# Performance work log

Measured on AMD Instinct MI355X. Metric: run time of the kernel, lower is better.

## Reference

```python
import jax, jax.numpy as jnp
import numpy as np

B, N, D, E = 4, 1024, 1024, 8
TOP_N = 2
THRESHOLD = 0.2
EPS = 1e-9
CAP_FACTOR = 2.0
MIN_EXPERT_CAPACITY = 4
H = int(D * 4 * 2 / 3)  # GEGLU hidden = 2730


def setup_inputs() -> dict:
    key = jax.random.key(0)
    ks = jax.random.split(key, 8)
    u = lambda k, shape, fan: jax.random.uniform(k, shape, jnp.float32, -1.0, 1.0) * (fan ** -0.5)
    return {
        "x": jax.random.normal(ks[0], (B, N, D), jnp.float32),
        "route_probs": jax.random.uniform(ks[1], (TOP_N, B, N), jnp.float32),
        "gate_w": u(ks[2], (D, E), D),
        "w1": u(ks[3], (E, D, 2 * H), 2 * H),
        "b1": u(ks[4], (E, 2 * H), 2 * H),
        "mult_bias": jnp.ones((E, H), jnp.float32),
        "w2": u(ks[5], (E, H, D), D),
        "b2": u(ks[6], (E, D), D),
    }


def reference(x, route_probs, gate_w, w1, b1, mult_bias, w2, b2):
    b, n, d = x.shape
    e = gate_w.shape[1]
    cap = max(min(n, int(n * CAP_FACTOR / e)), MIN_EXPERT_CAPACITY)  # 256

    # ---- top-n gating ----
    logits = jnp.einsum('bnd,de->bne', x, gate_w)
    raw_gates = jax.nn.softmax(logits, axis=-1)
    gate_vals, gate_idx = jax.lax.top_k(raw_gates, TOP_N)          # [b,n,k]
    gate_vals = jnp.moveaxis(gate_vals, -1, 0)                      # [k,b,n]
    gate_idx = jnp.moveaxis(gate_idx, -1, 0)                        # [k,b,n]
    one_hot_idx = jax.nn.one_hot(gate_idx, e, dtype=x.dtype)        # [k,b,n,e]

    denom = jnp.clip(gate_vals.sum(axis=0, keepdims=True), EPS)
    gate_vals = gate_vals / denom

    # route to expert k>0 with prob min(1, gate/threshold); expert 0 always routed
    should_route = route_probs < (gate_vals / THRESHOLD)
    should_route = should_route.at[0].set(True)
    mask = one_hot_idx * should_route[..., None].astype(x.dtype)    # [k,b,n,e]

    # exclusive cumsum over sequence dim -> position within each expert
    mask_cumsum = jnp.cumsum(mask, axis=2) - mask                   # [k,b,n,e]

    positions, masks = [], []
    prev_count = jnp.zeros((b, 1, e), x.dtype)
    for k in range(TOP_N):  # small fixed loop over top-n
        pos_e = (mask_cumsum[k] + prev_count) * mask[k]             # [b,n,e]
        mk = mask[k] * (pos_e < float(cap)).astype(x.dtype)
        prev_count = prev_count + mk.sum(axis=1, keepdims=True)
        positions.append(pos_e.sum(axis=-1))                        # [b,n]
        masks.append(mk)
    positions = jnp.stack(positions)                                # [k,b,n]
    mask = jnp.stack(masks)                                         # [k,b,n,e]

    mask_flat = mask.sum(axis=-1)                                   # [k,b,n] in {0,1}
    gates = gate_vals * mask_flat
    pos_one_hot = jax.nn.one_hot(positions.astype(jnp.int32), cap, dtype=x.dtype)  # [k,b,n,c]

    # combine tensor [b,n,e,c]; dispatch is its boolean support
    combine = jnp.einsum('kbn,kbne,kbnc->bnec', gates * mask_flat, one_hot_idx, pos_one_hot)
    dispatch = (combine > 0).astype(x.dtype)

    # ---- dispatch tokens to experts ----
    xe = jnp.einsum('bnd,bnec->ebcd', x, dispatch)                  # [e,b,c,d]

    # ---- per-expert GEGLU FFN (grouped GEMM) ----
    h = jnp.einsum('ebcd,edf->ebcf', xe, w1) + b1[:, None, None, :]
    val, gate = jnp.split(h, 2, axis=-1)
    act = jax.nn.gelu(gate, approximate=False) * val * mult_bias[:, None, None, :]
    out_e = jnp.einsum('ebch,ehd->ebcd', act, w2) + b2[:, None, None, :]

    # ---- combine ----
    out = jnp.einsum('ebcd,bnec->bnd', out_e, combine)
    return out


if __name__ == '__main__':
    inp = setup_inputs()
    o = reference(**inp)
    print(o.shape, o.dtype)
```

## Files before the change

### kernel.cpp

```cpp
#include <hip/hip_runtime.h>
#include <hip/hip_bf16.h>
#include <math.h>

#define B_ 4
#define N_ 1024
#define D_ 1024
#define E_ 8
#define H_ 2730
#define H2_ 5460
#define CAP_ 256
#define NTOK 4096
#define NSLOT 8192
#define NKT1 16
#define NKT2 43
#define NFG 22

typedef __attribute__((ext_vector_type(8))) short short8;
typedef __attribute__((ext_vector_type(4))) float f32x4;

__device__ __forceinline__ unsigned short f2bf(float f) {
    __hip_bfloat16 h = __float2bfloat16(f);
    return *reinterpret_cast<unsigned short*>(&h);
}
__device__ __forceinline__ float bf2f(unsigned short u) {
    unsigned x = ((unsigned)u) << 16;
    union { unsigned u; float f; } c; c.u = x; return c.f;
}

#define GLL16(g, l)                                                          \
    __builtin_amdgcn_global_load_lds(                                        \
        (const __attribute__((address_space(1))) void*)(g),                  \
        (__attribute__((address_space(3))) void*)(l), 16, 0, 0)

#define VMCNT4() asm volatile("s_waitcnt vmcnt(4)" ::: "memory")
#define VMCNT3() asm volatile("s_waitcnt vmcnt(3)" ::: "memory")
#define VMCNT0() asm volatile("s_waitcnt vmcnt(0)" ::: "memory")
#define SBAR()   __builtin_amdgcn_s_barrier()
#define SCHEDB() __builtin_amdgcn_sched_barrier(0)
#define MFMA16(a, b, c) __builtin_amdgcn_mfma_f32_16x16x32_bf16((a), (b), (c), 0, 0, 0)


__global__ __launch_bounds__(256) void k_cvt1(const float* __restrict__ w1,
                                              unsigned short* __restrict__ w1p) {
    const int fg = blockIdx.x;
    const int kt = blockIdx.y;
    const int e  = blockIdx.z;
    const float* w1e = w1 + (size_t)e * D_ * H2_;
    unsigned short* dst = w1p + (((size_t)((e * NFG + fg) * NKT1 + kt)) << 14);
#pragma unroll
    for (int i = 0; i < 8; ++i) {
        const int o = i * 256 + threadIdx.x;
        const int l = o & 63, n16 = (o >> 6) & 15, k32 = o >> 10;
        const int f = fg * 128 + ((n16 & 7) << 4) + (l & 15);
        const int k = kt * 64 + (k32 << 5) + ((l >> 4) << 3);
        ushort4 r0 = {0, 0, 0, 0}, r1 = {0, 0, 0, 0};
        if (f < H_) {
            const float* s = w1e + (size_t)k * H2_ + (n16 >= 8 ? H_ : 0) + f;
            r0.x = f2bf(s[0]);
            r0.y = f2bf(s[(size_t)H2_]);
            r0.z = f2bf(s[(size_t)2 * H2_]);
            r0.w = f2bf(s[(size_t)3 * H2_]);
            r1.x = f2bf(s[(size_t)4 * H2_]);
            r1.y = f2bf(s[(size_t)5 * H2_]);
            r1.z = f2bf(s[(size_t)6 * H2_]);
            r1.w = f2bf(s[(size_t)7 * H2_]);
        }
        *reinterpret_cast<ushort4*>(dst + (size_t)o * 8) = r0;
        *reinterpret_cast<ushort4*>(dst + (size_t)o * 8 + 4) = r1;
    }
}

__global__ __launch_bounds__(256) void k_cvt2(const float* __restrict__ w2,
                                              unsigned short* __restrict__ w2p) {
    const int kt = blockIdx.x;
    const int nt = blockIdx.y;
    const int e  = blockIdx.z;
    const float* w2e = w2 + (size_t)e * H_ * D_;
    unsigned short* dst = w2p + (((size_t)((e * 8 + nt) * NKT2 + kt)) << 13);
#pragma unroll
    for (int i = 0; i < 4; ++i) {
        const int o = i * 256 + threadIdx.x;
        const int l = o & 63, n16 = (o >> 6) & 7, k32 = o >> 9;
        const int d = nt * 128 + (n16 << 4) + (l & 15);
        const int f = kt * 64 + (k32 << 5) + ((l >> 4) << 3);
        const float* s = w2e + (size_t)f * D_ + d;
        ushort4 r0, r1;
        r0.x = (f + 0 < H_) ? f2bf(s[0]) : 0;
        r0.y = (f + 1 < H_) ? f2bf(s[(size_t)D_]) : 0;
        r0.z = (f + 2 < H_) ? f2bf(s[(size_t)2 * D_]) : 0;
        r0.w = (f + 3 < H_) ? f2bf(s[(size_t)3 * D_]) : 0;
        r1.x = (f + 4 < H_) ? f2bf(s[(size_t)4 * D_]) : 0;
        r1.y = (f + 5 < H_) ? f2bf(s[(size_t)5 * D_]) : 0;
        r1.z = (f + 6 < H_) ? f2bf(s[(size_t)6 * D_]) : 0;
        r1.w = (f + 7 < H_) ? f2bf(s[(size_t)7 * D_]) : 0;
        *reinterpret_cast<ushort4*>(dst + (size_t)o * 8) = r0;
        *reinterpret_cast<ushort4*>(dst + (size_t)o * 8 + 4) = r1;
    }
}

__global__ __launch_bounds__(256) void k_gate(const float* __restrict__ x,
                                              const float* __restrict__ route,
                                              const float* __restrict__ gw,
                                              int* __restrict__ tokE,
                                              float* __restrict__ tokG,
                                              int* __restrict__ tokR) {
    const int wave = threadIdx.x >> 6, lane = threadIdx.x & 63;
    const int t = blockIdx.x * 4 + wave;
    float acc[E_];
#pragma unroll
    for (int e = 0; e < E_; ++e) acc[e] = 0.f;
    const float* xr = x + (size_t)t * D_;
    for (int d = lane; d < D_; d += 64) {
        float xv = xr[d];
        const float* g = gw + d * E_;
#pragma unroll
        for (int e = 0; e < E_; ++e) acc[e] = fmaf(xv, g[e], acc[e]);
    }
#pragma unroll
    for (int e = 0; e < E_; ++e) {
#pragma unroll
        for (int off = 32; off; off >>= 1) acc[e] += __shfl_xor(acc[e], off);
    }
    if (lane == 0) {
        float m = acc[0];
#pragma unroll
        for (int e = 1; e < E_; ++e) m = fmaxf(m, acc[e]);
        float p[E_]; float s = 0.f;
#pragma unroll
        for (int e = 0; e < E_; ++e) { p[e] = expf(acc[e] - m); s += p[e]; }
        int i0 = 0; float v0 = p[0];
#pragma unroll
        for (int e = 1; e < E_; ++e) if (p[e] > v0) { v0 = p[e]; i0 = e; }
        int i1 = (i0 == 0) ? 1 : 0; float v1 = p[i1];
#pragma unroll
        for (int e = 0; e < E_; ++e) if (e != i0 && p[e] > v1) { v1 = p[e]; i1 = e; }
        float p0 = v0 / s, p1 = v1 / s;
        float denom = fmaxf(p0 + p1, 1e-9f);
        float g0 = p0 / denom, g1 = p1 / denom;
        int r1 = route[NTOK + t] < (g1 / 0.2f);
        tokE[t] = i0; tokE[NTOK + t] = i1;
        tokG[t] = g0; tokG[NTOK + t] = g1;
        tokR[t] = r1;
    }
}

__global__ __launch_bounds__(256) void k_pos(const int* __restrict__ tokE,
                                             const float* __restrict__ tokG,
                                             const int* __restrict__ tokR,
                                             int* __restrict__ sot,
                                             int* __restrict__ tos) {
    const int e = blockIdx.x & 7, b = blockIdx.x >> 3;
    const int t = threadIdx.x;
    __shared__ int sc[256];
    const int base_bt = b * N_ + t * 4;
    int m0[4], m1[4];
    int c0 = 0, c1 = 0;
#pragma unroll
    for (int i = 0; i < 4; ++i) {
        int bt = base_bt + i;
        m0[i] = (tokE[bt] == e) ? 1 : 0;
        m1[i] = ((tokE[NTOK + bt] == e) && tokR[bt]) ? 1 : 0;
        c0 += m0[i]; c1 += m1[i];
    }
    int packed = c0 | (c1 << 16);
    sc[t] = packed;
    __syncthreads();
    for (int off = 1; off < 256; off <<= 1) {
        int v = (t >= off) ? sc[t - off] : 0;
        __syncthreads();
        sc[t] += v;
        __syncthreads();
    }
    int incl = sc[t];
    int total = sc[255];
    int excl = incl - packed;
    int base0 = excl & 0xffff;
    int base1 = excl >> 16;
    int kept0 = min(total & 0xffff, CAP_);
#pragma unroll
    for (int i = 0; i < 4; ++i) {
        int bt = base_bt + i;
        if (m0[i]) {
            int pos = base0++;
            if (pos < CAP_ && tokG[bt] > 0.f) {
                int s = ((e * B_ + b) << 8) + pos;
                sot[bt] = s;
                tos[s] = bt;
            }
        }
        if (m1[i]) {
            int pos = (base1++) + kept0;
            if (pos < CAP_ && tokG[NTOK + bt] > 0.f) {
                int s = ((e * B_ + b) << 8) + pos;
                sot[NTOK + bt] = s;
                tos[s] = bt;
            }
        }
    }
}

__global__ __launch_bounds__(256) void k_disp(const float* __restrict__ x,
                                              const int* __restrict__ tos,
                                              unsigned short* __restrict__ xeP) {
    const int t = threadIdx.x;
    const int s = blockIdx.x * 2 + (t >> 7);
    const int q = t & 127;
    const int bt = tos[s];
    const int kt = q >> 3, k32 = (q >> 2) & 1, kq = q & 3;
    const int lane = (kq << 4) | (s & 15);
    const int m16 = (s >> 4) & 15;
    const int sgrp = s >> 8;
    unsigned short* dst = xeP + (((size_t)(sgrp * NKT1 + kt)) << 14) + (k32 << 13) + (m16 << 9) + lane * 8;
    ushort4 r0 = {0, 0, 0, 0}, r1 = {0, 0, 0, 0};
    if (bt >= 0) {
        const float4 v0 = *reinterpret_cast<const float4*>(x + ((size_t)bt << 10) + q * 8);
        const float4 v1 = *reinterpret_cast<const float4*>(x + ((size_t)bt << 10) + q * 8 + 4);
        r0.x = f2bf(v0.x); r0.y = f2bf(v0.y); r0.z = f2bf(v0.z); r0.w = f2bf(v0.w);
        r1.x = f2bf(v1.x); r1.y = f2bf(v1.y); r1.z = f2bf(v1.z); r1.w = f2bf(v1.w);
    }
    *reinterpret_cast<ushort4*>(dst) = r0;
    *reinterpret_cast<ushort4*>(dst + 4) = r1;
}

#define LDF(BUF, idx) (*reinterpret_cast<const short8*>(&BUF[(idx) * 512 + lane8]))

#define FFN1_MM03(AF0, AF1, AF2, AF3)                                         \
    do {                                                                      \
        acc[0][0]=MFMA16(AF0,bf0,acc[0][0]); acc[0][1]=MFMA16(AF0,bf1,acc[0][1]); \
        acc[0][2]=MFMA16(AF0,bf2,acc[0][2]); acc[0][3]=MFMA16(AF0,bf3,acc[0][3]); \
        acc[1][0]=MFMA16(AF1,bf0,acc[1][0]); acc[1][1]=MFMA16(AF1,bf1,acc[1][1]); \
        acc[1][2]=MFMA16(AF1,bf2,acc[1][2]); acc[1][3]=MFMA16(AF1,bf3,acc[1][3]); \
        acc[2][0]=MFMA16(AF2,bf0,acc[2][0]); acc[2][1]=MFMA16(AF2,bf1,acc[2][1]); \
        acc[2][2]=MFMA16(AF2,bf2,acc[2][2]); acc[2][3]=MFMA16(AF2,bf3,acc[2][3]); \
        acc[3][0]=MFMA16(AF3,bf0,acc[3][0]); acc[3][1]=MFMA16(AF3,bf1,acc[3][1]); \
        acc[3][2]=MFMA16(AF3,bf2,acc[3][2]); acc[3][3]=MFMA16(AF3,bf3,acc[3][3]); \
    } while (0)
#define FFN1_MM47(AF0, AF1, AF2, AF3)                                         \
    do {                                                                      \
        acc[4][0]=MFMA16(AF0,bf0,acc[4][0]); acc[4][1]=MFMA16(AF0,bf1,acc[4][1]); \
        acc[4][2]=MFMA16(AF0,bf2,acc[4][2]); acc[4][3]=MFMA16(AF0,bf3,acc[4][3]); \
        acc[5][0]=MFMA16(AF1,bf0,acc[5][0]); acc[5][1]=MFMA16(AF1,bf1,acc[5][1]); \
        acc[5][2]=MFMA16(AF1,bf2,acc[5][2]); acc[5][3]=MFMA16(AF1,bf3,acc[5][3]); \
        acc[6][0]=MFMA16(AF2,bf0,acc[6][0]); acc[6][1]=MFMA16(AF2,bf1,acc[6][1]); \
        acc[6][2]=MFMA16(AF2,bf2,acc[6][2]); acc[6][3]=MFMA16(AF2,bf3,acc[6][3]); \
        acc[7][0]=MFMA16(AF3,bf0,acc[7][0]); acc[7][1]=MFMA16(AF3,bf1,acc[7][1]); \
        acc[7][2]=MFMA16(AF3,bf2,acc[7][2]); acc[7][3]=MFMA16(AF3,bf3,acc[7][3]); \
    } while (0)

#define FFN1_KT(ARD, BRD, AWR, BWR, KTN, PF)                                  \
    do {                                                                      \
        const unsigned short* asn = abase + ((size_t)(KTN) << 14);            \
        const unsigned short* bsn = bbase + ((size_t)(KTN) << 14);            \
        short8 af0, af1, af2, af3, bf0, bf1, bf2, bf3;                        \
        SCHEDB(); VMCNT4(); SBAR(); SCHEDB();                                 \
        if (PF) {                                                             \
            GLL16(asn + woff + lane8, (char*)&AWR[woff]);                     \
            GLL16(asn + woff + 512 + lane8, (char*)&AWR[woff + 512]);         \
        }                                                                     \
        bf0 = LDF(BRD, bn0); bf1 = LDF(BRD, bn0 + 1);                         \
        bf2 = LDF(BRD, bn0 + 8); bf3 = LDF(BRD, bn0 + 9);                     \
        af0 = LDF(ARD, am0 + 0); af1 = LDF(ARD, am0 + 1);                     \
        af2 = LDF(ARD, am0 + 2); af3 = LDF(ARD, am0 + 3);                     \
        __builtin_amdgcn_s_setprio(1);                                        \
        FFN1_MM03(af0, af1, af2, af3);                                        \
        __builtin_amdgcn_s_setprio(0);                                        \
        if (PF) {                                                             \
            GLL16(bsn + woff + lane8, (char*)&BWR[woff]);                     \
            GLL16(bsn + woff + 512 + lane8, (char*)&BWR[woff + 512]);         \
        }                                                                     \
        af0 = LDF(ARD, am0 + 4); af1 = LDF(ARD, am0 + 5);                     \
        af2 = LDF(ARD, am0 + 6); af3 = LDF(ARD, am0 + 7);                     \
        __builtin_amdgcn_s_setprio(1);                                        \
        FFN1_MM47(af0, af1, af2, af3);                                        \
        __builtin_amdgcn_s_setprio(0);                                        \
        SCHEDB(); if (PF) { VMCNT4(); } else { VMCNT0(); } SBAR(); SCHEDB();  \
        if (PF) {                                                             \
            GLL16(asn + 8192 + woff + lane8, (char*)&AWR[8192 + woff]);       \
            GLL16(asn + 8192 + woff + 512 + lane8, (char*)&AWR[8192 + woff + 512]); \
        }                                                                     \
        bf0 = LDF(BRD, 16 + bn0); bf1 = LDF(BRD, 16 + bn0 + 1);               \
        bf2 = LDF(BRD, 16 + bn0 + 8); bf3 = LDF(BRD, 16 + bn0 + 9);           \
        af0 = LDF(ARD, 16 + am0 + 0); af1 = LDF(ARD, 16 + am0 + 1);           \
        af2 = LDF(ARD, 16 + am0 + 2); af3 = LDF(ARD, 16 + am0 + 3);           \
        __builtin_amdgcn_s_setprio(1);                                        \
        FFN1_MM03(af0, af1, af2, af3);                                        \
        __builtin_amdgcn_s_setprio(0);                                        \
        if (PF) {                                                             \
            GLL16(bsn + 8192 + woff + lane8, (char*)&BWR[8192 + woff]);       \
            GLL16(bsn + 8192 + woff + 512 + lane8, (char*)&BWR[8192 + woff + 512]); \
        }                                                                     \
        af0 = LDF(ARD, 16 + am0 + 4); af1 = LDF(ARD, 16 + am0 + 5);           \
        af2 = LDF(ARD, 16 + am0 + 6); af3 = LDF(ARD, 16 + am0 + 7);           \
        __builtin_amdgcn_s_setprio(1);                                        \
        FFN1_MM47(af0, af1, af2, af3);                                        \
        __builtin_amdgcn_s_setprio(0);                                        \
    } while (0)

__global__ __launch_bounds__(512) void k_ffn1(const unsigned short* __restrict__ xeP,
                                              const unsigned short* __restrict__ w1p,
                                              const float* __restrict__ b1,
                                              const float* __restrict__ mbias,
                                              unsigned short* __restrict__ actP) {
    const int wg = blockIdx.x;
    const int e = wg & 7;
    const int rem = wg >> 3;
    const int fg = rem >> 2;
    const int rt = rem & 3;
    const int sgrp = e * 4 + rt;

    __shared__ unsigned short Ab0[16384];
    __shared__ unsigned short Bb0[16384];
    __shared__ unsigned short Ab1[16384];
    __shared__ unsigned short Bb1[16384];

    const int tid = threadIdx.x, lane = tid & 63, w = tid >> 6;
    const int wm = w >> 2, wn = w & 3;
    const int lane8 = lane * 8;
    const int woff = w * 1024;
    const int am0 = wm * 8, bn0 = wn * 2;

    const unsigned short* abase = xeP + ((size_t)(sgrp * NKT1) << 14);
    const unsigned short* bbase = w1p + ((size_t)((e * NFG + fg) * NKT1) << 14);

    f32x4 acc[8][4];
#pragma unroll
    for (int i = 0; i < 8; ++i)
#pragma unroll
        for (int j = 0; j < 4; ++j) acc[i][j] = (f32x4)(0.f);

    GLL16(abase + woff + lane8, (char*)&Ab0[woff]);
    GLL16(abase + woff + 512 + lane8, (char*)&Ab0[woff + 512]);
    GLL16(bbase + woff + lane8, (char*)&Bb0[woff]);
    GLL16(bbase + woff + 512 + lane8, (char*)&Bb0[woff + 512]);
    GLL16(abase + 8192 + woff + lane8, (char*)&Ab0[8192 + woff]);
    GLL16(abase + 8192 + woff + 512 + lane8, (char*)&Ab0[8192 + woff + 512]);
    GLL16(bbase + 8192 + woff + lane8, (char*)&Bb0[8192 + woff]);
    GLL16(bbase + 8192 + woff + 512 + lane8, (char*)&Bb0[8192 + woff + 512]);

    for (int kt = 0; kt < NKT1; kt += 2) {
        FFN1_KT(Ab0, Bb0, Ab1, Bb1, kt + 1, 1);
        FFN1_KT(Ab1, Bb1, Ab0, Bb0, kt + 2, (kt + 2) < NKT1);
    }

    const float* b1e = b1 + (size_t)e * H2_;
    const float* mbe = mbias + (size_t)e * H_;
    const int colL = lane & 15, rq4 = (lane >> 4) * 4;
#pragma unroll
    for (int mi = 0; mi < 8; ++mi) {
        const int Rl = wm * 128 + mi * 16 + rq4;
#pragma unroll
        for (int vi = 0; vi < 2; ++vi) {
            const int f = fg * 128 + wn * 32 + vi * 16 + colL;
            if (f >= NKT2 * 64) continue;
            const bool real = f < H_;
            const float bv = real ? b1e[f] : 0.f;
            const float bg = real ? b1e[H_ + f] : 0.f;
            const float mv = real ? mbe[f] : 0.f;
            const int ktf = f >> 6, k32f = (f >> 5) & 1;
            const int lhi = ((f >> 3) & 3) << 4;
            const int bb = f & 7;
            const size_t cbase = ((size_t)(sgrp * NKT2 + ktf) << 14) + (k32f << 13);
#pragma unroll
            for (int j = 0; j < 4; ++j) {
                const int R = Rl + j;
                float a = 0.f;
                if (real) {
                    const float val = acc[mi][vi][j] + bv;
                    const float gt  = acc[mi][2 + vi][j] + bg;
                    a = 0.5f * gt * (1.f + erff(gt * 0.70710678118654752f)) * val * mv;
                }
                actP[cbase + ((R >> 4) << 9) + (size_t)((lhi | (R & 15)) * 8 + bb)] = f2bf(a);
            }
        }
    }
}

#define FFN2_MM03(AF0, AF1, AF2, AF3)                                         \
    do {                                                                      \
        acc[0][0]=MFMA16(AF0,bf0,acc[0][0]); acc[0][1]=MFMA16(AF0,bf1,acc[0][1]); \
        acc[1][0]=MFMA16(AF1,bf0,acc[1][0]); acc[1][1]=MFMA16(AF1,bf1,acc[1][1]); \
        acc[2][0]=MFMA16(AF2,bf0,acc[2][0]); acc[2][1]=MFMA16(AF2,bf1,acc[2][1]); \
        acc[3][0]=MFMA16(AF3,bf0,acc[3][0]); acc[3][1]=MFMA16(AF3,bf1,acc[3][1]); \
    } while (0)
#define FFN2_MM47(AF0, AF1, AF2, AF3)                                         \
    do {                                                                      \
        acc[4][0]=MFMA16(AF0,bf0,acc[4][0]); acc[4][1]=MFMA16(AF0,bf1,acc[4][1]); \
        acc[5][0]=MFMA16(AF1,bf0,acc[5][0]); acc[5][1]=MFMA16(AF1,bf1,acc[5][1]); \
        acc[6][0]=MFMA16(AF2,bf0,acc[6][0]); acc[6][1]=MFMA16(AF2,bf1,acc[6][1]); \
        acc[7][0]=MFMA16(AF3,bf0,acc[7][0]); acc[7][1]=MFMA16(AF3,bf1,acc[7][1]); \
    } while (0)

#define FFN2_KT(ARD, BRD, AWR, BWR, KTN, PF)                                  \
    do {                                                                      \
        const unsigned short* asn = abase + ((size_t)(KTN) << 14);            \
        const unsigned short* bsn = bbase + ((size_t)(KTN) << 13);            \
        short8 af0, af1, af2, af3, bf0, bf1;                                  \
        SCHEDB(); VMCNT3(); SBAR(); SCHEDB();                                 \
        if (PF) {                                                             \
            GLL16(asn + woff + lane8, (char*)&AWR[woff]);                     \
            GLL16(asn + woff + 512 + lane8, (char*)&AWR[woff + 512]);         \
        }                                                                     \
        bf0 = LDF(BRD, bn0); bf1 = LDF(BRD, bn0 + 1);                         \
        af0 = LDF(ARD, am0 + 0); af1 = LDF(ARD, am0 + 1);                     \
        af2 = LDF(ARD, am0 + 2); af3 = LDF(ARD, am0 + 3);                     \
        __builtin_amdgcn_s_setprio(1);                                        \
        FFN2_MM03(af0, af1, af2, af3);                                        \
        __builtin_amdgcn_s_setprio(0);                                        \
        if (PF) { GLL16(bsn + woffb + lane8, (char*)&BWR[woffb]); }           \
        af0 = LDF(ARD, am0 + 4); af1 = LDF(ARD, am0 + 5);                     \
        af2 = LDF(ARD, am0 + 6); af3 = LDF(ARD, am0 + 7);                     \
        __builtin_amdgcn_s_setprio(1);                                        \
        FFN2_MM47(af0, af1, af2, af3);                                        \
        __builtin_amdgcn_s_setprio(0);                                        \
        SCHEDB(); if (PF) { VMCNT3(); } else { VMCNT0(); } SBAR(); SCHEDB();  \
        if (PF) {                                                             \
            GLL16(asn + 8192 + woff + lane8, (char*)&AWR[8192 + woff]);       \
            GLL16(asn + 8192 + woff + 512 + lane8, (char*)&AWR[8192 + woff + 512]); \
        }                                                                     \
        bf0 = LDF(BRD, 8 + bn0); bf1 = LDF(BRD, 8 + bn0 + 1);                 \
        af0 = LDF(ARD, 16 + am0 + 0); af1 = LDF(ARD, 16 + am0 + 1);           \
        af2 = LDF(ARD, 16 + am0 + 2); af3 = LDF(ARD, 16 + am0 + 3);           \
        __builtin_amdgcn_s_setprio(1);                                        \
        FFN2_MM03(af0, af1, af2, af3);                                        \
        __builtin_amdgcn_s_setprio(0);                                        \
        if (PF) { GLL16(bsn + 4096 + woffb + lane8, (char*)&BWR[4096 + woffb]); } \
        af0 = LDF(ARD, 16 + am0 + 4); af1 = LDF(ARD, 16 + am0 + 5);           \
        af2 = LDF(ARD, 16 + am0 + 6); af3 = LDF(ARD, 16 + am0 + 7);           \
        __builtin_amdgcn_s_setprio(1);                                        \
        FFN2_MM47(af0, af1, af2, af3);                                        \
        __builtin_amdgcn_s_setprio(0);                                        \
    } while (0)

__global__ __launch_bounds__(512) void k_ffn2(const unsigned short* __restrict__ actP,
                                              const unsigned short* __restrict__ w2p,
                                              const float* __restrict__ b2,
                                              unsigned short* __restrict__ oute) {
    const int wg = blockIdx.x;
    const int e = wg & 7;
    const int rem = wg >> 3;
    const int nt = rem >> 2;
    const int mt = rem & 3;
    const int sgrp = e * 4 + mt;

    __shared__ unsigned short Ab0[16384];
    __shared__ unsigned short Bb0[8192];
    __shared__ unsigned short Ab1[16384];
    __shared__ unsigned short Bb1[8192];

    const int tid = threadIdx.x, lane = tid & 63, w = tid >> 6;
    const int wm = w >> 2, wn = w & 3;
    const int lane8 = lane * 8;
    const int woff = w * 1024;
    const int woffb = w * 512;
    const int am0 = wm * 8, bn0 = wn * 2;

    const unsigned short* abase = actP + ((size_t)(sgrp * NKT2) << 14);
    const unsigned short* bbase = w2p + ((size_t)((e * 8 + nt) * NKT2) << 13);

    f32x4 acc[8][2];
#pragma unroll
    for (int i = 0; i < 8; ++i)
#pragma unroll
        for (int j = 0; j < 2; ++j) acc[i][j] = (f32x4)(0.f);

    GLL16(abase + woff + lane8, (char*)&Ab0[woff]);
    GLL16(abase + woff + 512 + lane8, (char*)&Ab0[woff + 512]);
    GLL16(bbase + woffb + lane8, (char*)&Bb0[woffb]);
    GLL16(abase + 8192 + woff + lane8, (char*)&Ab0[8192 + woff]);
    GLL16(abase + 8192 + woff + 512 + lane8, (char*)&Ab0[8192 + woff + 512]);
    GLL16(bbase + 4096 + woffb + lane8, (char*)&Bb0[4096 + woffb]);

    for (int kt = 0; kt < NKT2 - 1; kt += 2) {
        FFN2_KT(Ab0, Bb0, Ab1, Bb1, kt + 1, 1);
        FFN2_KT(Ab1, Bb1, Ab0, Bb0, kt + 2, (kt + 2) < NKT2);
    }
    FFN2_KT(Ab0, Bb0, Ab1, Bb1, NKT2, 0);

    const float* b2e = b2 + (size_t)e * D_;
    const int colL = lane & 15, rq4 = (lane >> 4) * 4;
#pragma unroll
    for (int mi = 0; mi < 8; ++mi) {
#pragma unroll
        for (int vi = 0; vi < 2; ++vi) {
            const int d = nt * 128 + wn * 32 + vi * 16 + colL;
            const float bb2 = b2e[d];
#pragma unroll
            for (int j = 0; j < 4; ++j) {
                const int R = mt * 256 + wm * 128 + mi * 16 + rq4 + j;
                oute[((size_t)(e * 1024 + R) << 10) + d] = f2bf(acc[mi][vi][j] + bb2);
            }
        }
    }
}

__global__ __launch_bounds__(256) void k_comb(const unsigned short* __restrict__ oute,
                                              const int* __restrict__ sot,
                                              const float* __restrict__ tokG,
                                              float* __restrict__ out) {
    const int bt = blockIdx.x;
    const int t = threadIdx.x;
    const int s0 = sot[bt], s1 = sot[NTOK + bt];
    const float g0 = tokG[bt], g1 = tokG[NTOK + bt];
    float r0 = 0.f, r1 = 0.f, r2 = 0.f, r3 = 0.f;
    if (s0 >= 0) {
        const ushort4 v = *reinterpret_cast<const ushort4*>(oute + ((size_t)s0 << 10) + t * 4);
        r0 += g0 * bf2f(v.x); r1 += g0 * bf2f(v.y); r2 += g0 * bf2f(v.z); r3 += g0 * bf2f(v.w);
    }
    if (s1 >= 0) {
        const ushort4 v = *reinterpret_cast<const ushort4*>(oute + ((size_t)s1 << 10) + t * 4);
        r0 += g1 * bf2f(v.x); r1 += g1 * bf2f(v.y); r2 += g1 * bf2f(v.z); r3 += g1 * bf2f(v.w);
    }
    float4 o; o.x = r0; o.y = r1; o.z = r2; o.w = r3;
    *reinterpret_cast<float4*>(out + ((size_t)bt << 10) + t * 4) = o;
}

extern "C" void kernel_launch(void* const* d_in, const int* in_sizes, int n_in,
                              void* d_out, int out_size, void* d_ws, size_t ws_size,
                              hipStream_t stream) {
    const float* x     = (const float*)d_in[0];
    const float* route = (const float*)d_in[1];
    const float* gw    = (const float*)d_in[2];
    const float* w1    = (const float*)d_in[3];
    const float* b1    = (const float*)d_in[4];
    const float* mb    = (const float*)d_in[5];
    const float* w2    = (const float*)d_in[6];
    const float* b2    = (const float*)d_in[7];
    float* out = (float*)d_out;

    char* ws = (char*)d_ws;
    int*   tokE = (int*)(ws + 0);
    float* tokG = (float*)(ws + 32768);
    int*   tokR = (int*)(ws + 65536);
    int*   sot  = (int*)(ws + 81920);
    int*   tos  = (int*)(ws + 114688);
    unsigned short* xeP  = (unsigned short*)(ws + 147456);
    unsigned short* actP = (unsigned short*)(ws + 16924672);
    unsigned short* w1p  = (unsigned short*)(ws + 62013440);
    unsigned short* w2p  = (unsigned short*)(ws + 62013440);
    unsigned short* oute = (unsigned short*)(ws + 107102208);

    hipMemsetAsync(sot, 0xFF, 65536, stream);

    k_cvt1<<<dim3(NFG, NKT1, 8), 256, 0, stream>>>(w1, w1p);
    k_gate<<<NTOK / 4, 256, 0, stream>>>(x, route, gw, tokE, tokG, tokR);
    k_pos<<<E_ * B_, 256, 0, stream>>>(tokE, tokG, tokR, sot, tos);
    k_disp<<<NSLOT / 2, 256, 0, stream>>>(x, tos, xeP);
    k_ffn1<<<704, 512, 0, stream>>>(xeP, w1p, b1, mb, actP);
    k_cvt2<<<dim3(NKT2, 8, 8), 256, 0, stream>>>(w2, w2p);
    k_ffn2<<<256, 512, 0, stream>>>(actP, w2p, b2, oute);
    k_comb<<<NTOK, 256, 0, stream>>>(oute, sot, tokG, out);
}
```

Baseline: 325.6 us.

## Halve FFN GEMM M-tiles to 128 rows with 256-thread blocks

```diff
diff --git a/kernel.cpp b/kernel.cpp
--- a/kernel.cpp
+++ b/kernel.cpp
@@ -12,6 +12,7 @@
 #define NTOK 4096
 #define NSLOT 8192
 #define NKT1 16
+#define NK1T 32
 #define NKT2 43
 #define NFG 22
 
@@ -32,8 +33,6 @@
         (const __attribute__((address_space(1))) void*)(g),                  \
         (__attribute__((address_space(3))) void*)(l), 16, 0, 0)
 
-#define VMCNT4() asm volatile("s_waitcnt vmcnt(4)" ::: "memory")
-#define VMCNT3() asm volatile("s_waitcnt vmcnt(3)" ::: "memory")
 #define VMCNT0() asm volatile("s_waitcnt vmcnt(0)" ::: "memory")
 #define SBAR()   __builtin_amdgcn_s_barrier()
 #define SCHEDB() __builtin_amdgcn_sched_barrier(0)
@@ -224,79 +223,48 @@
 
 #define LDF(BUF, idx) (*reinterpret_cast<const short8*>(&BUF[(idx) * 512 + lane8]))
 
-#define FFN1_MM03(AF0, AF1, AF2, AF3)                                         \
+#define F1TILE(ARD, BRD, AWR, BWR, KTN, PF)                                   \
     do {                                                                      \
-        acc[0][0]=MFMA16(AF0,bf0,acc[0][0]); acc[0][1]=MFMA16(AF0,bf1,acc[0][1]); \
-        acc[0][2]=MFMA16(AF0,bf2,acc[0][2]); acc[0][3]=MFMA16(AF0,bf3,acc[0][3]); \
-        acc[1][0]=MFMA16(AF1,bf0,acc[1][0]); acc[1][1]=MFMA16(AF1,bf1,acc[1][1]); \
-        acc[1][2]=MFMA16(AF1,bf2,acc[1][2]); acc[1][3]=MFMA16(AF1,bf3,acc[1][3]); \
-        acc[2][0]=MFMA16(AF2,bf0,acc[2][0]); acc[2][1]=MFMA16(AF2,bf1,acc[2][1]); \
-        acc[2][2]=MFMA16(AF2,bf2,acc[2][2]); acc[2][3]=MFMA16(AF2,bf3,acc[2][3]); \
-        acc[3][0]=MFMA16(AF3,bf0,acc[3][0]); acc[3][1]=MFMA16(AF3,bf1,acc[3][1]); \
-        acc[3][2]=MFMA16(AF3,bf2,acc[3][2]); acc[3][3]=MFMA16(AF3,bf3,acc[3][3]); \
-    } while (0)
-#define FFN1_MM47(AF0, AF1, AF2, AF3)                                         \
-    do {                                                                      \
-        acc[4][0]=MFMA16(AF0,bf0,acc[4][0]); acc[4][1]=MFMA16(AF0,bf1,acc[4][1]); \
-        acc[4][2]=MFMA16(AF0,bf2,acc[4][2]); acc[4][3]=MFMA16(AF0,bf3,acc[4][3]); \
-        acc[5][0]=MFMA16(AF1,bf0,acc[5][0]); acc[5][1]=MFMA16(AF1,bf1,acc[5][1]); \
-        acc[5][2]=MFMA16(AF1,bf2,acc[5][2]); acc[5][3]=MFMA16(AF1,bf3,acc[5][3]); \
-        acc[6][0]=MFMA16(AF2,bf0,acc[6][0]); acc[6][1]=MFMA16(AF2,bf1,acc[6][1]); \
-        acc[6][2]=MFMA16(AF2,bf2,acc[6][2]); acc[6][3]=MFMA16(AF2,bf3,acc[6][3]); \
-        acc[7][0]=MFMA16(AF3,bf0,acc[7][0]); acc[7][1]=MFMA16(AF3,bf1,acc[7][1]); \
-        acc[7][2]=MFMA16(AF3,bf2,acc[7][2]); acc[7][3]=MFMA16(AF3,bf3,acc[7][3]); \
-    } while (0)
-
-#define FFN1_KT(ARD, BRD, AWR, BWR, KTN, PF)                                  \
-    do {                                                                      \
-        const unsigned short* asn = abase + ((size_t)(KTN) << 14);            \
-        const unsigned short* bsn = bbase + ((size_t)(KTN) << 14);            \
-        short8 af0, af1, af2, af3, bf0, bf1, bf2, bf3;                        \
-        SCHEDB(); VMCNT4(); SBAR(); SCHEDB();                                 \
+        VMCNT0(); SBAR(); SCHEDB();                                           \
         if (PF) {                                                             \
-            GLL16(asn + woff + lane8, (char*)&AWR[woff]);                     \
-            GLL16(asn + woff + 512 + lane8, (char*)&AWR[woff + 512]);         \
+            const unsigned short* as = abase + ((size_t)(KTN) << 13);         \
+            const unsigned short* bs = bbase + ((size_t)(KTN) << 13);         \
+            GLL16(as + t8, (char*)&AWR[wb]);                                  \
+            GLL16(as + 2048 + t8, (char*)&AWR[2048 + wb]);                    \
+            GLL16(bs + t8, (char*)&BWR[wb]);                                  \
+            GLL16(bs + 2048 + t8, (char*)&BWR[2048 + wb]);                    \
+            GLL16(bs + 4096 + t8, (char*)&BWR[4096 + wb]);                    \
+            GLL16(bs + 6144 + t8, (char*)&BWR[6144 + wb]);                    \
         }                                                                     \
-        bf0 = LDF(BRD, bn0); bf1 = LDF(BRD, bn0 + 1);                         \
-        bf2 = LDF(BRD, bn0 + 8); bf3 = LDF(BRD, bn0 + 9);                     \
+        SCHEDB();                                                             \
+        short8 af0, af1, af2, af3, b0, b1, b2, b3, b4, b5, b6, b7;            \
         af0 = LDF(ARD, am0 + 0); af1 = LDF(ARD, am0 + 1);                     \
         af2 = LDF(ARD, am0 + 2); af3 = LDF(ARD, am0 + 3);                     \
+        b0 = LDF(BRD, bn0 + 0); b1 = LDF(BRD, bn0 + 1);                       \
+        b2 = LDF(BRD, bn0 + 2); b3 = LDF(BRD, bn0 + 3);                       \
+        b4 = LDF(BRD, 8 + bn0 + 0); b5 = LDF(BRD, 8 + bn0 + 1);               \
+        b6 = LDF(BRD, 8 + bn0 + 2); b7 = LDF(BRD, 8 + bn0 + 3);               \
         __builtin_amdgcn_s_setprio(1);                                        \
-        FFN1_MM03(af0, af1, af2, af3);                                        \
-        __builtin_amdgcn_s_setprio(0);                                        \
-        if (PF) {                                                             \
-            GLL16(bsn + woff + lane8, (char*)&BWR[woff]);                     \
-            GLL16(bsn + woff + 512 + lane8, (char*)&BWR[woff + 512]);         \
-        }                                                                     \
-        af0 = LDF(ARD, am0 + 4); af1 = LDF(ARD, am0 + 5);                     \
-        af2 = LDF(ARD, am0 + 6); af3 = LDF(ARD, am0 + 7);                     \
-        __builtin_amdgcn_s_setprio(1);                                        \
-        FFN1_MM47(af0, af1, af2, af3);                                        \
-        __builtin_amdgcn_s_setprio(0);                                        \
-        SCHEDB(); if (PF) { VMCNT4(); } else { VMCNT0(); } SBAR(); SCHEDB();  \
-        if (PF) {                                                             \
-            GLL16(asn + 8192 + woff + lane8, (char*)&AWR[8192 + woff]);       \
-            GLL16(asn + 8192 + woff + 512 + lane8, (char*)&AWR[8192 + woff + 512]); \
-        }                                                                     \
-        bf0 = LDF(BRD, 16 + bn0); bf1 = LDF(BRD, 16 + bn0 + 1);               \
-        bf2 = LDF(BRD, 16 + bn0 + 8); bf3 = LDF(BRD, 16 + bn0 + 9);           \
-        af0 = LDF(ARD, 16 + am0 + 0); af1 = LDF(ARD, 16 + am0 + 1);           \
-        af2 = LDF(ARD, 16 + am0 + 2); af3 = LDF(ARD, 16 + am0 + 3);           \
-        __builtin_amdgcn_s_setprio(1);                                        \
-        FFN1_MM03(af0, af1, af2, af3);                                        \
-        __builtin_amdgcn_s_setprio(0);                                        \
-        if (PF) {                                                             \
-            GLL16(bsn + 8192 + woff + lane8, (char*)&BWR[8192 + woff]);       \
-            GLL16(bsn + 8192 + woff + 512 + lane8, (char*)&BWR[8192 + woff + 512]); \
-        }                                                                     \
-        af0 = LDF(ARD, 16 + am0 + 4); af1 = LDF(ARD, 16 + am0 + 5);           \
-        af2 = LDF(ARD, 16 + am0 + 6); af3 = LDF(ARD, 16 + am0 + 7);           \
-        __builtin_amdgcn_s_setprio(1);                                        \
-        FFN1_MM47(af0, af1, af2, af3);                                        \
+        acc[0][0]=MFMA16(af0,b0,acc[0][0]); acc[0][1]=MFMA16(af0,b1,acc[0][1]); \
+        acc[0][2]=MFMA16(af0,b2,acc[0][2]); acc[0][3]=MFMA16(af0,b3,acc[0][3]); \
+        acc[0][4]=MFMA16(af0,b4,acc[0][4]); acc[0][5]=MFMA16(af0,b5,acc[0][5]); \
+        acc[0][6]=MFMA16(af0,b6,acc[0][6]); acc[0][7]=MFMA16(af0,b7,acc[0][7]); \
+        acc[1][0]=MFMA16(af1,b0,acc[1][0]); acc[1][1]=MFMA16(af1,b1,acc[1][1]); \
+        acc[1][2]=MFMA16(af1,b2,acc[1][2]); acc[1][3]=MFMA16(af1,b3,acc[1][3]); \
+        acc[1][4]=MFMA16(af1,b4,acc[1][4]); acc[1][5]=MFMA16(af1,b5,acc[1][5]); \
+        acc[1][6]=MFMA16(af1,b6,acc[1][6]); acc[1][7]=MFMA16(af1,b7,acc[1][7]); \
+        acc[2][0]=MFMA16(af2,b0,acc[2][0]); acc[2][1]=MFMA16(af2,b1,acc[2][1]); \
+        acc[2][2]=MFMA16(af2,b2,acc[2][2]); acc[2][3]=MFMA16(af2,b3,acc[2][3]); \
+        acc[2][4]=MFMA16(af2,b4,acc[2][4]); acc[2][5]=MFMA16(af2,b5,acc[2][5]); \
+        acc[2][6]=MFMA16(af2,b6,acc[2][6]); acc[2][7]=MFMA16(af2,b7,acc[2][7]); \
+        acc[3][0]=MFMA16(af3,b0,acc[3][0]); acc[3][1]=MFMA16(af3,b1,acc[3][1]); \
+        acc[3][2]=MFMA16(af3,b2,acc[3][2]); acc[3][3]=MFMA16(af3,b3,acc[3][3]); \
+        acc[3][4]=MFMA16(af3,b4,acc[3][4]); acc[3][5]=MFMA16(af3,b5,acc[3][5]); \
+        acc[3][6]=MFMA16(af3,b6,acc[3][6]); acc[3][7]=MFMA16(af3,b7,acc[3][7]); \
         __builtin_amdgcn_s_setprio(0);                                        \
     } while (0)
 
-__global__ __launch_bounds__(512) void k_ffn1(const unsigned short* __restrict__ xeP,
+__global__ __launch_bounds__(256) void k_ffn1(const unsigned short* __restrict__ xeP,
                                               const unsigned short* __restrict__ w1p,
                                               const float* __restrict__ b1,
                                               const float* __restrict__ mbias,
@@ -304,53 +272,55 @@
     const int wg = blockIdx.x;
     const int e = wg & 7;
     const int rem = wg >> 3;
-    const int fg = rem >> 2;
-    const int rt = rem & 3;
-    const int sgrp = e * 4 + rt;
-
-    __shared__ unsigned short Ab0[16384];
-    __shared__ unsigned short Bb0[16384];
-    __shared__ unsigned short Ab1[16384];
-    __shared__ unsigned short Bb1[16384];
+    const int fg = rem >> 3;
+    const int rt = rem & 7;
+    const int sgrp = e * 4 + (rt >> 1);
+    const int half = rt & 1;
+
+    __shared__ unsigned short Ab0[4096];
+    __shared__ unsigned short Bb0[8192];
+    __shared__ unsigned short Ab1[4096];
+    __shared__ unsigned short Bb1[8192];
 
     const int tid = threadIdx.x, lane = tid & 63, w = tid >> 6;
-    const int wm = w >> 2, wn = w & 3;
+    const int wm = w >> 1, wn = w & 1;
     const int lane8 = lane * 8;
-    const int woff = w * 1024;
-    const int am0 = wm * 8, bn0 = wn * 2;
-
-    const unsigned short* abase = xeP + ((size_t)(sgrp * NKT1) << 14);
+    const int t8 = tid * 8;
+    const int wb = w * 512;
+    const int am0 = wm * 4, bn0 = wn * 4;
+
+    const unsigned short* abase = xeP + ((size_t)(sgrp * NKT1) << 14) + half * 4096;
     const unsigned short* bbase = w1p + ((size_t)((e * NFG + fg) * NKT1) << 14);
 
-    f32x4 acc[8][4];
-#pragma unroll
-    for (int i = 0; i < 8; ++i)
-#pragma unroll
-        for (int j = 0; j < 4; ++j) acc[i][j] = (f32x4)(0.f);
-
-    GLL16(abase + woff + lane8, (char*)&Ab0[woff]);
-    GLL16(abase + woff + 512 + lane8, (char*)&Ab0[woff + 512]);
-    GLL16(bbase + woff + lane8, (char*)&Bb0[woff]);
-    GLL16(bbase + woff + 512 + lane8, (char*)&Bb0[woff + 512]);
-    GLL16(abase + 8192 + woff + lane8, (char*)&Ab0[8192 + woff]);
-    GLL16(abase + 8192 + woff + 512 + lane8, (char*)&Ab0[8192 + woff + 512]);
-    GLL16(bbase + 8192 + woff + lane8, (char*)&Bb0[8192 + woff]);
-    GLL16(bbase + 8192 + woff + 512 + lane8, (char*)&Bb0[8192 + woff + 512]);
-
-    for (int kt = 0; kt < NKT1; kt += 2) {
-        FFN1_KT(Ab0, Bb0, Ab1, Bb1, kt + 1, 1);
-        FFN1_KT(Ab1, Bb1, Ab0, Bb0, kt + 2, (kt + 2) < NKT1);
+    f32x4 acc[4][8];
+#pragma unroll
+    for (int i = 0; i < 4; ++i)
+#pragma unroll
+        for (int j = 0; j < 8; ++j) acc[i][j] = (f32x4)(0.f);
+
+    GLL16(abase + t8, (char*)&Ab0[wb]);
+    GLL16(abase + 2048 + t8, (char*)&Ab0[2048 + wb]);
+    GLL16(bbase + t8, (char*)&Bb0[wb]);
+    GLL16(bbase + 2048 + t8, (char*)&Bb0[2048 + wb]);
+    GLL16(bbase + 4096 + t8, (char*)&Bb0[4096 + wb]);
+    GLL16(bbase + 6144 + t8, (char*)&Bb0[6144 + wb]);
+
+    for (int kt = 0; kt < NK1T; kt += 2) {
+        F1TILE(Ab0, Bb0, Ab1, Bb1, kt + 1, 1);
+        F1TILE(Ab1, Bb1, Ab0, Bb0, kt + 2, (kt + 2) < NK1T);
     }
 
     const float* b1e = b1 + (size_t)e * H2_;
     const float* mbe = mbias + (size_t)e * H_;
     const int colL = lane & 15, rq4 = (lane >> 4) * 4;
 #pragma unroll
-    for (int mi = 0; mi < 8; ++mi) {
-        const int Rl = wm * 128 + mi * 16 + rq4;
-#pragma unroll
-        for (int vi = 0; vi < 2; ++vi) {
-            const int f = fg * 128 + wn * 32 + vi * 16 + colL;
+    for (int mi = 0; mi < 4; ++mi) {
+        const int rowbase = rt * 128 + wm * 64 + mi * 16;
+        const int sg2 = e * 4 + (rowbase >> 8);
+        const int m16w = (rowbase >> 4) & 15;
+#pragma unroll
+        for (int v = 0; v < 4; ++v) {
+            const int f = fg * 128 + wn * 64 + v * 16 + colL;
             if (f >= NKT2 * 64) continue;
             const bool real = f < H_;
             const float bv = real ? b1e[f] : 0.f;
@@ -359,135 +329,128 @@
             const int ktf = f >> 6, k32f = (f >> 5) & 1;
             const int lhi = ((f >> 3) & 3) << 4;
             const int bb = f & 7;
-            const size_t cbase = ((size_t)(sgrp * NKT2 + ktf) << 14) + (k32f << 13);
+            const size_t cbase = ((size_t)(sg2 * NKT2 + ktf) << 14) + (k32f << 13) + (m16w << 9);
 #pragma unroll
             for (int j = 0; j < 4; ++j) {
-                const int R = Rl + j;
                 float a = 0.f;
                 if (real) {
-                    const float val = acc[mi][vi][j] + bv;
-                    const float gt  = acc[mi][2 + vi][j] + bg;
+                    const float val = acc[mi][v][j] + bv;
+                    const float gt  = acc[mi][4 + v][j] + bg;
                     a = 0.5f * gt * (1.f + erff(gt * 0.70710678118654752f)) * val * mv;
                 }
-                actP[cbase + ((R >> 4) << 9) + (size_t)((lhi | (R & 15)) * 8 + bb)] = f2bf(a);
+                actP[cbase + (size_t)((lhi | (rq4 + j)) * 8 + bb)] = f2bf(a);
             }
         }
     }
 }
 
-#define FFN2_MM03(AF0, AF1, AF2, AF3)                                         \
+#define F2TILE(ARD, BRD, AWR, BWR, KTN, PF)                                   \
     do {                                                                      \
-        acc[0][0]=MFMA16(AF0,bf0,acc[0][0]); acc[0][1]=MFMA16(AF0,bf1,acc[0][1]); \
-        acc[1][0]=MFMA16(AF1,bf0,acc[1][0]); acc[1][1]=MFMA16(AF1,bf1,acc[1][1]); \
-        acc[2][0]=MFMA16(AF2,bf0,acc[2][0]); acc[2][1]=MFMA16(AF2,bf1,acc[2][1]); \
-        acc[3][0]=MFMA16(AF3,bf0,acc[3][0]); acc[3][1]=MFMA16(AF3,bf1,acc[3][1]); \
-    } while (0)
-#define FFN2_MM47(AF0, AF1, AF2, AF3)                                         \
-    do {                                                                      \
-        acc[4][0]=MFMA16(AF0,bf0,acc[4][0]); acc[4][1]=MFMA16(AF0,bf1,acc[4][1]); \
-        acc[5][0]=MFMA16(AF1,bf0,acc[5][0]); acc[5][1]=MFMA16(AF1,bf1,acc[5][1]); \
-        acc[6][0]=MFMA16(AF2,bf0,acc[6][0]); acc[6][1]=MFMA16(AF2,bf1,acc[6][1]); \
-        acc[7][0]=MFMA16(AF3,bf0,acc[7][0]); acc[7][1]=MFMA16(AF3,bf1,acc[7][1]); \
-    } while (0)
-
-#define FFN2_KT(ARD, BRD, AWR, BWR, KTN, PF)                                  \
-    do {                                                                      \
-        const unsigned short* asn = abase + ((size_t)(KTN) << 14);            \
-        const unsigned short* bsn = bbase + ((size_t)(KTN) << 13);            \
-        short8 af0, af1, af2, af3, bf0, bf1;                                  \
-        SCHEDB(); VMCNT3(); SBAR(); SCHEDB();                                 \
+        VMCNT0(); SBAR(); SCHEDB();                                           \
         if (PF) {                                                             \
-            GLL16(asn + woff + lane8, (char*)&AWR[woff]);                     \
-            GLL16(asn + woff + 512 + lane8, (char*)&AWR[woff + 512]);         \
+            const unsigned short* as = abase + ((size_t)(KTN) << 14);         \
+            const unsigned short* bs = bbase + ((size_t)(KTN) << 13);         \
+            GLL16(as + t8, (char*)&AWR[wb]);                                  \
+            GLL16(as + 2048 + t8, (char*)&AWR[2048 + wb]);                    \
+            GLL16(as + 8192 + t8, (char*)&AWR[4096 + wb]);                    \
+            GLL16(as + 10240 + t8, (char*)&AWR[6144 + wb]);                   \
+            GLL16(bs + t8, (char*)&BWR[wb]);                                  \
+            GLL16(bs + 2048 + t8, (char*)&BWR[2048 + wb]);                    \
+            GLL16(bs + 4096 + t8, (char*)&BWR[4096 + wb]);                    \
+            GLL16(bs + 6144 + t8, (char*)&BWR[6144 + wb]);                    \
         }                                                                     \
-        bf0 = LDF(BRD, bn0); bf1 = LDF(BRD, bn0 + 1);                         \
-        af0 = LDF(ARD, am0 + 0); af1 = LDF(ARD, am0 + 1);                     \
-        af2 = LDF(ARD, am0 + 2); af3 = LDF(ARD, am0 + 3);                     \
+        SCHEDB();                                                             \
+        short8 a0, a1, a2, a3, b0, b1, b2, b3;                                \
+        a0 = LDF(ARD, am0 + 0); a1 = LDF(ARD, am0 + 1);                       \
+        a2 = LDF(ARD, am0 + 2); a3 = LDF(ARD, am0 + 3);                       \
+        b0 = LDF(BRD, bn0 + 0); b1 = LDF(BRD, bn0 + 1);                       \
+        b2 = LDF(BRD, bn0 + 2); b3 = LDF(BRD, bn0 + 3);                       \
         __builtin_amdgcn_s_setprio(1);                                        \
-        FFN2_MM03(af0, af1, af2, af3);                                        \
+        acc[0][0]=MFMA16(a0,b0,acc[0][0]); acc[0][1]=MFMA16(a0,b1,acc[0][1]); \
+        acc[0][2]=MFMA16(a0,b2,acc[0][2]); acc[0][3]=MFMA16(a0,b3,acc[0][3]); \
+        acc[1][0]=MFMA16(a1,b0,acc[1][0]); acc[1][1]=MFMA16(a1,b1,acc[1][1]); \
+        acc[1][2]=MFMA16(a1,b2,acc[1][2]); acc[1][3]=MFMA16(a1,b3,acc[1][3]); \
+        acc[2][0]=MFMA16(a2,b0,acc[2][0]); acc[2][1]=MFMA16(a2,b1,acc[2][1]); \
+        acc[2][2]=MFMA16(a2,b2,acc[2][2]); acc[2][3]=MFMA16(a2,b3,acc[2][3]); \
+        acc[3][0]=MFMA16(a3,b0,acc[3][0]); acc[3][1]=MFMA16(a3,b1,acc[3][1]); \
+        acc[3][2]=MFMA16(a3,b2,acc[3][2]); acc[3][3]=MFMA16(a3,b3,acc[3][3]); \
         __builtin_amdgcn_s_setprio(0);                                        \
-        if (PF) { GLL16(bsn + woffb + lane8, (char*)&BWR[woffb]); }           \
-        af0 = LDF(ARD, am0 + 4); af1 = LDF(ARD, am0 + 5);                     \
-        af2 = LDF(ARD, am0 + 6); af3 = LDF(ARD, am0 + 7);                     \
+        a0 = LDF(ARD, 8 + am0 + 0); a1 = LDF(ARD, 8 + am0 + 1);               \
+        a2 = LDF(ARD, 8 + am0 + 2); a3 = LDF(ARD, 8 + am0 + 3);               \
+        b0 = LDF(BRD, 8 + bn0 + 0); b1 = LDF(BRD, 8 + bn0 + 1);               \
+        b2 = LDF(BRD, 8 + bn0 + 2); b3 = LDF(BRD, 8 + bn0 + 3);               \
         __builtin_amdgcn_s_setprio(1);                                        \
-        FFN2_MM47(af0, af1, af2, af3);                                        \
-        __builtin_amdgcn_s_setprio(0);                                        \
-        SCHEDB(); if (PF) { VMCNT3(); } else { VMCNT0(); } SBAR(); SCHEDB();  \
-        if (PF) {                                                             \
-            GLL16(asn + 8192 + woff + lane8, (char*)&AWR[8192 + woff]);       \
-            GLL16(asn + 8192 + woff + 512 + lane8, (char*)&AWR[8192 + woff + 512]); \
-        }                                                                     \
-        bf0 = LDF(BRD, 8 + bn0); bf1 = LDF(BRD, 8 + bn0 + 1);                 \
-        af0 = LDF(ARD, 16 + am0 + 0); af1 = LDF(ARD, 16 + am0 + 1);           \
-        af2 = LDF(ARD, 16 + am0 + 2); af3 = LDF(ARD, 16 + am0 + 3);           \
-        __builtin_amdgcn_s_setprio(1);                                        \
-        FFN2_MM03(af0, af1, af2, af3);                                        \
-        __builtin_amdgcn_s_setprio(0);                                        \
-        if (PF) { GLL16(bsn + 4096 + woffb + lane8, (char*)&BWR[4096 + woffb]); } \
-        af0 = LDF(ARD, 16 + am0 + 4); af1 = LDF(ARD, 16 + am0 + 5);           \
-        af2 = LDF(ARD, 16 + am0 + 6); af3 = LDF(ARD, 16 + am0 + 7);           \
-        __builtin_amdgcn_s_setprio(1);                                        \
-        FFN2_MM47(af0, af1, af2, af3);                                        \
+        acc[0][0]=MFMA16(a0,b0,acc[0][0]); acc[0][1]=MFMA16(a0,b1,acc[0][1]); \
+        acc[0][2]=MFMA16(a0,b2,acc[0][2]); acc[0][3]=MFMA16(a0,b3,acc[0][3]); \
+        acc[1][0]=MFMA16(a1,b0,acc[1][0]); acc[1][1]=MFMA16(a1,b1,acc[1][1]); \
+        acc[1][2]=MFMA16(a1,b2,acc[1][2]); acc[1][3]=MFMA16(a1,b3,acc[1][3]); \
+        acc[2][0]=MFMA16(a2,b0,acc[2][0]); acc[2][1]=MFMA16(a2,b1,acc[2][1]); \
+        acc[2][2]=MFMA16(a2,b2,acc[2][2]); acc[2][3]=MFMA16(a2,b3,acc[2][3]); \
+        acc[3][0]=MFMA16(a3,b0,acc[3][0]); acc[3][1]=MFMA16(a3,b1,acc[3][1]); \
+        acc[3][2]=MFMA16(a3,b2,acc[3][2]); acc[3][3]=MFMA16(a3,b3,acc[3][3]); \
         __builtin_amdgcn_s_setprio(0);                                        \
     } while (0)
 
-__global__ __launch_bounds__(512) void k_ffn2(const unsigned short* __restrict__ actP,
+__global__ __launch_bounds__(256) void k_ffn2(const unsigned short* __restrict__ actP,
                                               const unsigned short* __restrict__ w2p,
                                               const float* __restrict__ b2,
                                               unsigned short* __restrict__ oute) {
     const int wg = blockIdx.x;
     const int e = wg & 7;
     const int rem = wg >> 3;
-    const int nt = rem >> 2;
-    const int mt = rem & 3;
-    const int sgrp = e * 4 + mt;
-
-    __shared__ unsigned short Ab0[16384];
+    const int nt = rem >> 3;
+    const int mt = rem & 7;
+    const int sgrp = e * 4 + (mt >> 1);
+    const int half = mt & 1;
+
+    __shared__ unsigned short Ab0[8192];
     __shared__ unsigned short Bb0[8192];
-    __shared__ unsigned short Ab1[16384];
+    __shared__ unsigned short Ab1[8192];
     __shared__ unsigned short Bb1[8192];
 
     const int tid = threadIdx.x, lane = tid & 63, w = tid >> 6;
-    const int wm = w >> 2, wn = w & 3;
+    const int wm = w >> 1, wn = w & 1;
     const int lane8 = lane * 8;
-    const int woff = w * 1024;
-    const int woffb = w * 512;
-    const int am0 = wm * 8, bn0 = wn * 2;
-
-    const unsigned short* abase = actP + ((size_t)(sgrp * NKT2) << 14);
+    const int t8 = tid * 8;
+    const int wb = w * 512;
+    const int am0 = wm * 4, bn0 = wn * 4;
+
+    const unsigned short* abase = actP + ((size_t)(sgrp * NKT2) << 14) + half * 4096;
     const unsigned short* bbase = w2p + ((size_t)((e * 8 + nt) * NKT2) << 13);
 
-    f32x4 acc[8][2];
-#pragma unroll
-    for (int i = 0; i < 8; ++i)
-#pragma unroll
-        for (int j = 0; j < 2; ++j) acc[i][j] = (f32x4)(0.f);
-
-    GLL16(abase + woff + lane8, (char*)&Ab0[woff]);
-    GLL16(abase + woff + 512 + lane8, (char*)&Ab0[woff + 512]);
-    GLL16(bbase + woffb + lane8, (char*)&Bb0[woffb]);
-    GLL16(abase + 8192 + woff + lane8, (char*)&Ab0[8192 + woff]);
-    GLL16(abase + 8192 + woff + 512 + lane8, (char*)&Ab0[8192 + woff + 512]);
-    GLL16(bbase + 4096 + woffb + lane8, (char*)&Bb0[4096 + woffb]);
+    f32x4 acc[4][4];
+#pragma unroll
+    for (int i = 0; i < 4; ++i)
+#pragma unroll
+        for (int j = 0; j < 4; ++j) acc[i][j] = (f32x4)(0.f);
+
+    GLL16(abase + t8, (char*)&Ab0[wb]);
+    GLL16(abase + 2048 + t8, (char*)&Ab0[2048 + wb]);
+    GLL16(abase + 8192 + t8, (char*)&Ab0[4096 + wb]);
+    GLL16(abase + 10240 + t8, (char*)&Ab0[6144 + wb]);
+    GLL16(bbase + t8, (char*)&Bb0[wb]);
+    GLL16(bbase + 2048 + t8, (char*)&Bb0[2048 + wb]);
+    GLL16(bbase + 4096 + t8, (char*)&Bb0[4096 + wb]);
+    GLL16(bbase + 6144 + t8, (char*)&Bb0[6144 + wb]);
 
     for (int kt = 0; kt < NKT2 - 1; kt += 2) {
-        FFN2_KT(Ab0, Bb0, Ab1, Bb1, kt + 1, 1);
-        FFN2_KT(Ab1, Bb1, Ab0, Bb0, kt + 2, (kt + 2) < NKT2);
-    }
-    FFN2_KT(Ab0, Bb0, Ab1, Bb1, NKT2, 0);
+        F2TILE(Ab0, Bb0, Ab1, Bb1, kt + 1, 1);
+        F2TILE(Ab1, Bb1, Ab0, Bb0, kt + 2, (kt + 2) < NKT2);
+    }
+    F2TILE(Ab0, Bb0, Ab1, Bb1, NKT2, 0);
 
     const float* b2e = b2 + (size_t)e * D_;
     const int colL = lane & 15, rq4 = (lane >> 4) * 4;
 #pragma unroll
-    for (int mi = 0; mi < 8; ++mi) {
-#pragma unroll
-        for (int vi = 0; vi < 2; ++vi) {
-            const int d = nt * 128 + wn * 32 + vi * 16 + colL;
+    for (int mi = 0; mi < 4; ++mi) {
+#pragma unroll
+        for (int nf = 0; nf < 4; ++nf) {
+            const int d = nt * 128 + wn * 64 + nf * 16 + colL;
             const float bb2 = b2e[d];
 #pragma unroll
             for (int j = 0; j < 4; ++j) {
-                const int R = mt * 256 + wm * 128 + mi * 16 + rq4 + j;
-                oute[((size_t)(e * 1024 + R) << 10) + d] = f2bf(acc[mi][vi][j] + bb2);
+                const int R = mt * 128 + wm * 64 + mi * 16 + rq4 + j;
+                oute[((size_t)(e * 1024 + R) << 10) + d] = f2bf(acc[mi][nf][j] + bb2);
             }
         }
     }
@@ -545,8 +508,8 @@
     k_gate<<<NTOK / 4, 256, 0, stream>>>(x, route, gw, tokE, tokG, tokR);
     k_pos<<<E_ * B_, 256, 0, stream>>>(tokE, tokG, tokR, sot, tos);
     k_disp<<<NSLOT / 2, 256, 0, stream>>>(x, tos, xeP);
-    k_ffn1<<<704, 512, 0, stream>>>(xeP, w1p, b1, mb, actP);
+    k_ffn1<<<1408, 256, 0, stream>>>(xeP, w1p, b1, mb, actP);
     k_cvt2<<<dim3(NKT2, 8, 8), 256, 0, stream>>>(w2, w2p);
-    k_ffn2<<<256, 512, 0, stream>>>(actP, w2p, b2, oute);
+    k_ffn2<<<512, 256, 0, stream>>>(actP, w2p, b2, oute);
     k_comb<<<NTOK, 256, 0, stream>>>(oute, sot, tokG, out);
 }
```

Result: slower. 399.2 us (+22.6%).
